# Kernel optimization log

Measured on AMD Instinct MI355X. Metric: run time of the kernel, lower is better.

Reference implementation:

```python
import jax, jax.numpy as jnp
import numpy as np

B, S, H = 2, 1024, 2048
HEADS = 16
QC = 1536      # q_compressed_dim
KVC = 512      # kv_compressed_dim
ROPE = 64      # qk_rope_dim
NOPE = H // HEADS  # 128, non-rope head dim
VH = 128       # v_head_dim
INTER = 1408   # MoE intermediate dim
NSH = 2        # shared experts
NRT = 8        # routed experts
TOPK = 2
EPS = 1e-6


def setup_inputs() -> dict:
    key = jax.random.key(0)
    ks = jax.random.split(key, 16)

    def w(k, shape, scale=0.02):
        return jax.random.normal(k, shape, jnp.float32) * scale

    return {
        "x": jax.random.normal(ks[0], (B, S, H), jnp.float32),
        "freq": jax.random.uniform(ks[1], (S, ROPE // 2), jnp.float32, 0.0, 2.0 * np.pi),
        "mask": jnp.zeros((S, S), jnp.float32),
        "w_attn_norm": jnp.ones((H,), jnp.float32),
        "w_ffn_norm": jnp.ones((H,), jnp.float32),
        "W_dq": w(ks[2], (H, QC)),
        "q_c_norm": jnp.ones((QC,), jnp.float32),
        "W_uq": w(ks[3], (QC, HEADS * (NOPE + ROPE))),
        "W_dkv": w(ks[4], (H, KVC + ROPE)),
        "kv_c_norm": jnp.ones((KVC,), jnp.float32),
        "W_ukv": w(ks[5], (KVC, HEADS * (NOPE + VH))),
        "W_o": w(ks[6], (HEADS * VH, H)),
        "W_r": w(ks[7], (H, NRT)),
        "Ws_gate": w(ks[8], (NSH, H, INTER)),
        "Ws_up": w(ks[9], (NSH, H, INTER)),
        "Ws_down": w(ks[10], (NSH, INTER, H)),
        "We_gate": w(ks[11], (NRT, H, INTER)),
        "We_up": w(ks[12], (NRT, H, INTER)),
        "We_down": w(ks[13], (NRT, INTER, H)),
    }


def rmsnorm(x, w):
    return x * jax.lax.rsqrt(jnp.mean(x * x, axis=-1, keepdims=True) + EPS) * w


def rope_apply(x, cos, sin):
    # x: [..., S, D]; cos/sin: [S, D/2], interleaved-pair rotation
    x1 = x[..., 0::2]
    x2 = x[..., 1::2]
    return jnp.stack([x1 * cos - x2 * sin, x1 * sin + x2 * cos], axis=-1).reshape(x.shape)


def _experts(t, Wg, Wu, Wd):
    # t: [T,H]; W*: [E,H,I]/[E,I,H] -> [E,T,H], SwiGLU per expert
    hid = jax.nn.silu(jnp.einsum('th,ehi->eti', t, Wg)) * jnp.einsum('th,ehi->eti', t, Wu)
    return jnp.einsum('eti,eih->eth', hid, Wd)


def reference(x, freq, mask, w_attn_norm, w_ffn_norm, W_dq, q_c_norm, W_uq, W_dkv,
              kv_c_norm, W_ukv, W_o, W_r, Ws_gate, Ws_up, Ws_down,
              We_gate, We_up, We_down):
    Bb, Ss, Hh = x.shape
    cos = jnp.cos(freq)
    sin = jnp.sin(freq)

    # ---- MLA attention (pre-norm) ----
    h = rmsnorm(x, w_attn_norm)
    cq = rmsnorm(h @ W_dq, q_c_norm)                              # [B,S,QC]
    q = (cq @ W_uq).reshape(Bb, Ss, HEADS, NOPE + ROPE).transpose(0, 2, 1, 3)
    q_nope, q_rope = q[..., :NOPE], q[..., NOPE:]
    q_rope = rope_apply(q_rope, cos, sin)                          # [B,Hh,S,ROPE]

    ckv = h @ W_dkv                                               # [B,S,KVC+ROPE]
    kv_c = rmsnorm(ckv[..., :KVC], kv_c_norm)
    k_rope = rope_apply(ckv[..., KVC:], cos, sin)                  # [B,S,ROPE] shared over heads
    kv = (kv_c @ W_ukv).reshape(Bb, Ss, HEADS, NOPE + VH).transpose(0, 2, 1, 3)
    k_nope, v = kv[..., :NOPE], kv[..., NOPE:]

    scale = 1.0 / np.sqrt(NOPE + ROPE)
    scores = (jnp.einsum('bhsd,bhtd->bhst', q_nope, k_nope)
              + jnp.einsum('bhsd,btd->bhst', q_rope, k_rope)) * scale + mask
    attn = jax.nn.softmax(scores, axis=-1)
    attn_out = jnp.einsum('bhst,bhtd->bshd', attn, v).reshape(Bb, Ss, HEADS * VH) @ W_o
    x = x + attn_out

    # ---- DeepSeekMoE FFN (pre-norm) ----
    t = rmsnorm(x, w_ffn_norm).reshape(Bb * Ss, Hh)
    shared = _experts(t, Ws_gate, Ws_up, Ws_down).sum(axis=0)      # [T,H]
    probs = jax.nn.softmax(t @ W_r, axis=-1)                       # [T,E]
    vals, idx = jax.lax.top_k(probs, TOPK)
    weights = (jax.nn.one_hot(idx, NRT, dtype=t.dtype) * vals[..., None]).sum(axis=1)  # [T,E]
    routed = jnp.einsum('eth,te->th', _experts(t, We_gate, We_up, We_down), weights)
    return x + (shared + routed).reshape(Bb, Ss, Hh)
```

## Files before the change

kernel.cpp:

```cpp
#include <hip/hip_runtime.h>

typedef __bf16 bf16;
typedef _Float16 f16;
typedef unsigned short u16;
typedef __bf16 bf16x8 __attribute__((ext_vector_type(8)));
typedef _Float16 f16x8 __attribute__((ext_vector_type(8)));
typedef unsigned short u16x8 __attribute__((ext_vector_type(8)));
typedef float f32x4 __attribute__((ext_vector_type(4)));

#define TOK   2048
#define SEQ   1024
#define HIDD  2048
#define NHEADS 16
#define QCD   1536
#define KVCD  512
#define ROPED 64
#define NOPED 128
#define QDIM  192
#define VHD   128
#define KVD   576
#define KVDP  640
#define INTERD 1408
#define GUD   2816
#define RMS_EPS 1e-6f
#define SPS   64.0f
#define OSC   (1.0f/4096.0f)

__device__ inline void split64(float v, f16& h, f16& l) {
    v *= SPS; h = (f16)v; l = (f16)(v - (float)h);
}

__device__ inline void gl_lds16(const void* g, void* l) {
    __builtin_amdgcn_global_load_lds(
        (const __attribute__((address_space(1))) void*)g,
        (__attribute__((address_space(3))) void*)l,
        16, 0, 0);
}

#define WAITN(N) asm volatile("s_waitcnt vmcnt(" #N ")" ::: "memory")

__global__ __launch_bounds__(256) void tconv_ex3_kernel(const float* __restrict__ gate,
                                                        const float* __restrict__ up,
                                                        const float* __restrict__ down,
                                                        bf16* __restrict__ dGU,
                                                        bf16* __restrict__ dD) {
    const float* src; bf16* dst; int K, N, rowMul, rowAdd;
    if (blockIdx.z == 0)      { src = gate; dst = dGU; K = HIDD;   N = INTERD; rowMul = 2; rowAdd = 0; }
    else if (blockIdx.z == 1) { src = up;   dst = dGU; K = HIDD;   N = INTERD; rowMul = 2; rowAdd = 1; }
    else                      { src = down; dst = dD;  K = INTERD; N = HIDD;   rowMul = 1; rowAdd = 0; }
    int nb = blockIdx.x * 32, kb = blockIdx.y * 32;
    if (nb >= N || kb >= K) return;
    __shared__ float tile[32][33];
    int tx = threadIdx.x & 31, ty = threadIdx.x >> 5;
#pragma unroll
    for (int i = 0; i < 32; i += 8)
        tile[ty + i][tx] = src[(long)(kb + ty + i) * N + nb + tx];
    __syncthreads();
#pragma unroll
    for (int i = 0; i < 32; i += 8) {
        int n = nb + ty + i;
        dst[(long)(n * rowMul + rowAdd) * K + kb + tx] = (bf16)tile[tx][ty + i];
    }
}

__global__ __launch_bounds__(256) void tconv_guall_kernel(const float* __restrict__ gate,
                                                          const float* __restrict__ up,
                                                          bf16* __restrict__ dstAll) {
    int e = blockIdx.z >> 1, isUp = blockIdx.z & 1;
    const float* src = (isUp ? up : gate) + (size_t)e * HIDD * INTERD;
    bf16* dst = dstAll + (size_t)e * GUD * HIDD;
    int nb = blockIdx.x * 32, kb = blockIdx.y * 32;
    __shared__ float tile[32][33];
    int tx = threadIdx.x & 31, ty = threadIdx.x >> 5;
#pragma unroll
    for (int i = 0; i < 32; i += 8)
        tile[ty + i][tx] = src[(long)(kb + ty + i) * INTERD + nb + tx];
    __syncthreads();
#pragma unroll
    for (int i = 0; i < 32; i += 8) {
        int n = nb + ty + i;
        dst[(long)(n * 2 + isUp) * HIDD + kb + tx] = (bf16)tile[tx][ty + i];
    }
}

__global__ __launch_bounds__(256) void tconv_downall_kernel(const float* __restrict__ down,
                                                            bf16* __restrict__ dstAll) {
    int e = blockIdx.z;
    const float* src = down + (size_t)e * INTERD * HIDD;
    bf16* dst = dstAll + (size_t)e * HIDD * INTERD;
    int nb = blockIdx.x * 32, kb = blockIdx.y * 32;
    __shared__ float tile[32][33];
    int tx = threadIdx.x & 31, ty = threadIdx.x >> 5;
#pragma unroll
    for (int i = 0; i < 32; i += 8)
        tile[ty + i][tx] = src[(long)(kb + ty + i) * HIDD + nb + tx];
    __syncthreads();
#pragma unroll
    for (int i = 0; i < 32; i += 8)
        dst[(long)(nb + ty + i) * INTERD + kb + tx] = (bf16)tile[tx][ty + i];
}

__global__ __launch_bounds__(256) void tconv3h_kernel(const float* __restrict__ src,
                                                      f16* __restrict__ dst,
                                                      int K, int N, int Npad) {
    __shared__ float tile[32][33];
    int nb = blockIdx.x * 32, kb = blockIdx.y * 32;
    int tx = threadIdx.x & 31, ty = threadIdx.x >> 5;
#pragma unroll
    for (int i = 0; i < 32; i += 8) {
        int k = kb + ty + i, n = nb + tx;
        tile[ty + i][tx] = (k < K && n < N) ? src[(long)k * N + n] : 0.f;
    }
    __syncthreads();
#pragma unroll
    for (int i = 0; i < 32; i += 8) {
        int n = nb + ty + i, k = kb + tx;
        if (n < Npad && k < K) {
            f16 h, l; split64(tile[tx][ty + i], h, l);
            long base = (long)n * (3 * K) + k;
            dst[base] = h; dst[base + K] = l; dst[base + 2 * K] = h;
        }
    }
}

template<int F16, int TM, int TN>
__global__ __launch_bounds__(256) void gemm_bt_kernel(
    const u16* __restrict__ A, const u16* __restrict__ B, void* __restrict__ Cv,
    const float* __restrict__ aux, const int* __restrict__ idx,
    const int* __restrict__ cntPtr,
    int K, int lda, int ldb, int ldc,
    long sA, long sB, long sC,
    int mode, int auxLd, float osc)
{
    constexpr int AM = TM / 32;
    constexpr int AN = TN / 32;
    constexpr int NBUF = (TM + TN > 192) ? 2 : 3;
    constexpr int PF = NBUF - 1;
    constexpr int L = TM / 32 + TN / 32;
    __shared__ u16 As[NBUF][TM * 64];
    __shared__ u16 Bs[NBUF][TN * 64];
    const int bn = blockIdx.x, bm = blockIdx.y, z = blockIdx.z;
    int cnt = 1 << 30;
    if (cntPtr) {
        cnt = cntPtr[z];
        int pad = (cnt + TM - 1) & ~(TM - 1);
        if (bm * TM >= pad) return;
    }
    const int tid = threadIdx.x, lane = tid & 63, w = tid >> 6;
    const int wm = w >> 1, wn = w & 1;
    const int lr = lane & 15;
    const int srow = lane >> 3, c16 = lane & 7;
    const u16* Ab = A + (long)z * sA + (long)bm * TM * lda;
    const u16* Bb = B + (long)z * sB + (long)bn * TN * ldb;
    f32x4 acc[AM][AN] = {};

    const bool aidx = (idx != nullptr && mode == 7);
    int iperm[4];
    if (aidx) {
#pragma unroll
        for (int i = 0; i < TM / 32; i++) {
            int r = bm * TM + i * 32 + w * 8 + srow;
            int v = idx[(long)z * TOK + r];
            iperm[i] = (r < cnt) ? v : 0;
        }
    }

    auto stage = [&](int buf, int k0) {
#pragma unroll
        for (int i = 0; i < TM / 32; i++) {
            int rb = i * 32 + w * 8;
            int row = rb + srow;
            int gc = ((c16 ^ (row & 7)) << 3);
            const u16* src = aidx ? (A + (long)iperm[i] * lda + k0 + gc)
                                  : (Ab + (long)row * lda + k0 + gc);
            gl_lds16(src, &As[buf][rb * 64]);
        }
#pragma unroll
        for (int i = 0; i < TN / 32; i++) {
            int rb = i * 32 + w * 8;
            int row = rb + srow;
            int gc = ((c16 ^ (row & 7)) << 3);
            gl_lds16(&Bb[(long)row * ldb + k0 + gc], &Bs[buf][rb * 64]);
        }
    };
    auto compute = [&](int cur) {
#pragma unroll
        for (int ks = 0; ks < 2; ks++) {
            u16x8 af[AM], bfr[AN];
#pragma unroll
            for (int mi = 0; mi < AM; mi++) {
                int row = wm * (TM / 2) + mi * 16 + lr;
                int cg = (ks * 4 + (lane >> 4)) ^ (row & 7);
                af[mi] = *(const u16x8*)&As[cur][row * 64 + cg * 8];
            }
#pragma unroll
            for (int ni = 0; ni < AN; ni++) {
                int row = wn * (TN / 2) + ni * 16 + lr;
                int cg = (ks * 4 + (lane >> 4)) ^ (row & 7);
                bfr[ni] = *(const u16x8*)&Bs[cur][row * 64 + cg * 8];
            }
#pragma unroll
            for (int mi = 0; mi < AM; mi++)
#pragma unroll
                for (int ni = 0; ni < AN; ni++) {
                    if constexpr (F16)
                        acc[mi][ni] = __builtin_amdgcn_mfma_f32_16x16x32_f16(
                            __builtin_bit_cast(f16x8, af[mi]),
                            __builtin_bit_cast(f16x8, bfr[ni]), acc[mi][ni], 0, 0, 0);
                    else
                        acc[mi][ni] = __builtin_amdgcn_mfma_f32_16x16x32_bf16(
                            __builtin_bit_cast(bf16x8, af[mi]),
                            __builtin_bit_cast(bf16x8, bfr[ni]), acc[mi][ni], 0, 0, 0);
                }
        }
    };

    const int nk = K >> 6;
#pragma unroll
    for (int p = 0; p < PF; ++p) if (p < nk) stage(p, p << 6);

    if constexpr (PF == 2) {
        for (int t = 0; t < nk; ++t) {
            if (t + PF < nk) stage((t + PF) % NBUF, (t + PF) << 6);
            const int inflight = (nk - 1 - t < PF) ? (nk - 1 - t) : PF;
            if (inflight >= 2) {
                if constexpr (L == 4) WAITN(8); else WAITN(12);
            } else if (inflight == 1) {
                if constexpr (L == 4) WAITN(4); else WAITN(6);
            } else {
                WAITN(0);
            }
            __builtin_amdgcn_s_barrier();
            __builtin_amdgcn_sched_barrier(0);
            compute(t % NBUF);
            __builtin_amdgcn_s_barrier();
        }
    } else {
        for (int t = 0; t < nk; ++t) {
            if (t + 1 < nk) stage((t + 1) & 1, (t + 1) << 6);
            if (t + 1 < nk) WAITN(8);
            else            WAITN(0);
            __builtin_amdgcn_s_barrier();
            __builtin_amdgcn_sched_barrier(0);
            compute(t & 1);
            __builtin_amdgcn_s_barrier();
        }
    }

    const int r0 = (lane >> 4) << 2;
    const int rowBase = bm * TM + wm * (TM / 2);
    const int colBase = bn * TN + wn * (TN / 2);
#pragma unroll
    for (int mi = 0; mi < AM; mi++) {
#pragma unroll
        for (int ni = 0; ni < AN; ni++) {
#pragma unroll
            for (int r = 0; r < 4; r++) {
                int row = rowBase + mi * 16 + r0 + r;
                int col = colBase + ni * 16 + lr;
                float val = acc[mi][ni][r] * osc;
                long ci = (long)z * sC + (long)row * ldc + col;
                if (mode == 0) {
                    ((float*)Cv)[ci] = val;
                } else if (mode == 2) {
                    ((float*)Cv)[ci] = val + aux[(long)row * auxLd + col];
                } else if (mode == 3) {
                    float s = aux ? aux[(long)row * auxLd] : 1.f;
                    ((float*)Cv)[ci] += s * val;
                } else if (mode == 5) {
                    if (row < cnt) {
                        int tok = idx[(long)z * TOK + row];
                        atomicAdd(&((float*)Cv)[(long)tok * ldc + col],
                                  aux[(long)tok * auxLd + z] * val);
                    }
                } else if (mode == 7) {
                    float other = __shfl_xor(val, 1, 64);
                    if (!(lane & 1)) {
                        float g = val, u = other;
                        ((bf16*)Cv)[(long)z * sC + (long)row * auxLd + (col >> 1)] =
                            (bf16)(g / (1.f + expf(-g)) * u);
                    }
                } else {
                    f16 h = (f16)val; f16 l = (f16)(val - (float)h);
                    ((f16*)Cv)[ci] = h; ((f16*)Cv)[ci + auxLd] = h; ((f16*)Cv)[ci + 2 * auxLd] = l;
                }
            }
        }
    }
}

__global__ __launch_bounds__(256) void rmsnorm_kernel(const float* __restrict__ in,
                                                      const float* __restrict__ w,
                                                      bf16* __restrict__ outB,
                                                      float* __restrict__ copyOut, int C) {
    long row = blockIdx.x;
    const float* r = in + row * C;
    float ss = 0.f;
    for (int i = threadIdx.x; i < C; i += 256) { float v = r[i]; ss += v * v; }
    for (int off = 32; off > 0; off >>= 1) ss += __shfl_down(ss, off, 64);
    __shared__ float red[5];
    int lane = threadIdx.x & 63, wv = threadIdx.x >> 6;
    if (lane == 0) red[wv] = ss;
    __syncthreads();
    if (threadIdx.x == 0) red[4] = rsqrtf((red[0] + red[1] + red[2] + red[3]) / C + RMS_EPS);
    __syncthreads();
    float sc = red[4];
    for (int i = threadIdx.x; i < C; i += 256) {
        outB[row * C + i] = (bf16)(r[i] * sc * w[i]);
        if (copyOut) copyOut[row * C + i] = r[i];
    }
}

__global__ __launch_bounds__(256) void rmsnorm3h_kernel(const float* __restrict__ in,
                                                        const float* __restrict__ w,
                                                        f16* __restrict__ out3, int C) {
    long row = blockIdx.x;
    const float* r = in + row * C;
    float ss = 0.f;
    for (int i = threadIdx.x; i < C; i += 256) { float v = r[i]; ss += v * v; }
    for (int off = 32; off > 0; off >>= 1) ss += __shfl_down(ss, off, 64);
    __shared__ float red[5];
    int lane = threadIdx.x & 63, wv = threadIdx.x >> 6;
    if (lane == 0) red[wv] = ss;
    __syncthreads();
    if (threadIdx.x == 0) red[4] = rsqrtf((red[0] + red[1] + red[2] + red[3]) / C + RMS_EPS);
    __syncthreads();
    float sc = red[4];
    f16* o = out3 + row * (3L * C);
    for (int i = threadIdx.x; i < C; i += 256) {
        f16 h, l; split64(r[i] * sc * w[i], h, l);
        o[i] = h; o[C + i] = h; o[2 * C + i] = l;
    }
}

__global__ __launch_bounds__(256) void kvsplit3h_kernel(const float* __restrict__ ckv,
                                                        const float* __restrict__ nrm,
                                                        const float* __restrict__ freq,
                                                        f16* __restrict__ kvc3,
                                                        float* __restrict__ krope) {
    int t = blockIdx.x; int s = t & (SEQ - 1);
    const float* r = ckv + (long)t * KVDP;
    float ss = 0.f;
    for (int i = threadIdx.x; i < KVCD; i += 256) { float v = r[i]; ss += v * v; }
    for (int off = 32; off > 0; off >>= 1) ss += __shfl_down(ss, off, 64);
    __shared__ float red[5];
    int lane = threadIdx.x & 63, wv = threadIdx.x >> 6;
    if (lane == 0) red[wv] = ss;
    __syncthreads();
    if (threadIdx.x == 0) red[4] = rsqrtf((red[0] + red[1] + red[2] + red[3]) / KVCD + RMS_EPS);
    __syncthreads();
    float sc = red[4];
    f16* o = kvc3 + (long)t * (3 * KVCD);
    for (int i = threadIdx.x; i < KVCD; i += 256) {
        f16 h, l; split64(r[i] * sc * nrm[i], h, l);
        o[i] = h; o[KVCD + i] = h; o[2 * KVCD + i] = l;
    }
    if (threadIdx.x < 32) {
        int i = threadIdx.x;
        float f = freq[s * 32 + i], c = cosf(f), sn = sinf(f);
        float x1 = r[KVCD + 2 * i], x2 = r[KVCD + 2 * i + 1];
        krope[(long)t * ROPED + 2 * i]     = x1 * c - x2 * sn;
        krope[(long)t * ROPED + 2 * i + 1] = x1 * sn + x2 * c;
    }
}

__global__ __launch_bounds__(256) void build_q3h_kernel(const float* __restrict__ qpre,
                                                        const float* __restrict__ freq,
                                                        f16* __restrict__ q3) {
    int t = blockIdx.x; int b = t >> 10, s = t & (SEQ - 1);
    for (int idx = threadIdx.x; idx < NHEADS * 96; idx += 256) {
        int h = idx / 96, j = idx % 96;
        const float* qrow = qpre + (long)t * 3072 + h * QDIM;
        f16* dst = q3 + ((long)(b * NHEADS + h) * SEQ + s) * (3 * QDIM);
        if (j < 64) {
            int d = 2 * j;
#pragma unroll
            for (int u = 0; u < 2; u++) {
                f16 hh, ll; split64(qrow[d + u], hh, ll);
                dst[d + u] = hh; dst[QDIM + d + u] = hh; dst[2 * QDIM + d + u] = ll;
            }
        } else {
            int i = j - 64;
            float f = freq[s * 32 + i], c = cosf(f), sn = sinf(f);
            float x1 = qrow[NOPED + 2 * i], x2 = qrow[NOPED + 2 * i + 1];
            float v0 = x1 * c - x2 * sn, v1 = x1 * sn + x2 * c;
            int d = NOPED + 2 * i;
            f16 h0, l0, h1, l1; split64(v0, h0, l0); split64(v1, h1, l1);
            dst[d] = h0; dst[QDIM + d] = h0; dst[2 * QDIM + d] = l0;
            dst[d + 1] = h1; dst[QDIM + d + 1] = h1; dst[2 * QDIM + d + 1] = l1;
        }
    }
}

__global__ __launch_bounds__(256) void build_k3h_kernel(const float* __restrict__ kv,
                                                        const float* __restrict__ krope,
                                                        f16* __restrict__ k3,
                                                        f16* __restrict__ v3T) {
    int t = blockIdx.x; int b = t >> 10, s = t & (SEQ - 1);
    const float* kvrow = kv + (long)t * 4096;
    const float* kr = krope + (long)t * ROPED;
    for (int idx = threadIdx.x; idx < NHEADS * 96; idx += 256) {
        int h = idx / 96, j = idx % 96;
        f16* dst = k3 + ((long)(b * NHEADS + h) * SEQ + s) * (3 * QDIM);
        float v0, v1; int d;
        if (j < 64) { d = 2 * j; v0 = kvrow[h * 256 + d]; v1 = kvrow[h * 256 + d + 1]; }
        else { int i = j - 64; d = NOPED + 2 * i; v0 = kr[2 * i]; v1 = kr[2 * i + 1]; }
        f16 h0, l0, h1, l1; split64(v0, h0, l0); split64(v1, h1, l1);
        dst[d] = h0; dst[QDIM + d] = l0; dst[2 * QDIM + d] = h0;
        dst[d + 1] = h1; dst[QDIM + d + 1] = l1; dst[2 * QDIM + d + 1] = h1;
    }
    for (int idx = threadIdx.x; idx < NHEADS * VHD; idx += 256) {
        int h = idx >> 7, d = idx & 127;
        f16 hh, ll; split64(kvrow[h * 256 + NOPED + d], hh, ll);
        long base = ((long)(b * NHEADS + h) * VHD + d) * (3 * SEQ) + s;
        v3T[base] = hh; v3T[base + SEQ] = ll; v3T[base + 2 * SEQ] = hh;
    }
}

__global__ __launch_bounds__(256) void softmax3h_kernel(const float* __restrict__ scores,
                                                        const float* __restrict__ mask,
                                                        f16* __restrict__ P3, float scale) {
    int s = blockIdx.x, h = blockIdx.y;
    const float* row  = scores + ((long)h * SEQ + s) * SEQ;
    const float* mrow = mask + (long)s * SEQ;
    f16* prow = P3 + ((long)h * SEQ + s) * (3 * SEQ);
    float v[4]; float m = -1e30f;
#pragma unroll
    for (int j = 0; j < 4; j++) {
        int i = threadIdx.x + j * 256;
        v[j] = row[i] * scale + mrow[i];
        m = fmaxf(m, v[j]);
    }
    for (int off = 32; off > 0; off >>= 1) m = fmaxf(m, __shfl_down(m, off, 64));
    __shared__ float redm[5], reds[5];
    int lane = threadIdx.x & 63, wv = threadIdx.x >> 6;
    if (lane == 0) redm[wv] = m;
    __syncthreads();
    if (threadIdx.x == 0) redm[4] = fmaxf(fmaxf(redm[0], redm[1]), fmaxf(redm[2], redm[3]));
    __syncthreads();
    float M = redm[4];
    float sum = 0.f;
#pragma unroll
    for (int j = 0; j < 4; j++) { v[j] = expf(v[j] - M); sum += v[j]; }
    for (int off = 32; off > 0; off >>= 1) sum += __shfl_down(sum, off, 64);
    if (lane == 0) reds[wv] = sum;
    __syncthreads();
    if (threadIdx.x == 0) reds[4] = reds[0] + reds[1] + reds[2] + reds[3];
    __syncthreads();
    float inv = 1.f / reds[4];
#pragma unroll
    for (int j = 0; j < 4; j++) {
        int i = threadIdx.x + j * 256;
        f16 hh, ll; split64(v[j] * inv, hh, ll);
        prow[i] = hh; prow[SEQ + i] = hh; prow[2 * SEQ + i] = ll;
    }
}

__global__ void zero_counts_kernel(int* counts) {
    if (threadIdx.x < 8) counts[threadIdx.x] = 0;
}

__global__ __launch_bounds__(64) void router_kernel(const float* __restrict__ x2,
                                                    const float* __restrict__ wffn,
                                                    const float* __restrict__ Wr,
                                                    float* __restrict__ wts,
                                                    int* __restrict__ perm,
                                                    int* __restrict__ counts) {
    int t = blockIdx.x; int lane = threadIdx.x;
    const float* r = x2 + (long)t * HIDD;
    float ss = 0.f;
    for (int k = lane; k < HIDD; k += 64) { float v = r[k]; ss += v * v; }
    for (int off = 32; off > 0; off >>= 1) ss += __shfl_down(ss, off, 64);
    float sc = rsqrtf(__shfl(ss, 0, 64) / HIDD + RMS_EPS);
    float acc[8] = {0, 0, 0, 0, 0, 0, 0, 0};
    for (int k = lane; k < HIDD; k += 64) {
        float tv = r[k] * sc * wffn[k];
        const float* wr = Wr + (long)k * 8;
#pragma unroll
        for (int e = 0; e < 8; e++) acc[e] += tv * wr[e];
    }
#pragma unroll
    for (int e = 0; e < 8; e++)
        for (int off = 32; off > 0; off >>= 1) acc[e] += __shfl_down(acc[e], off, 64);
    if (lane == 0) {
        float m = acc[0];
#pragma unroll
        for (int e = 1; e < 8; e++) m = fmaxf(m, acc[e]);
        float p[8]; float se = 0.f;
#pragma unroll
        for (int e = 0; e < 8; e++) { p[e] = expf(acc[e] - m); se += p[e]; }
        float inv = 1.f / se;
        int i1 = 0; float v1 = p[0];
        for (int e = 1; e < 8; e++) if (p[e] > v1) { v1 = p[e]; i1 = e; }
        int i2 = -1; float v2 = -1.f;
        for (int e = 0; e < 8; e++) if (e != i1 && p[e] > v2) { v2 = p[e]; i2 = e; }
#pragma unroll
        for (int e = 0; e < 8; e++)
            wts[(long)t * 8 + e] = (e == i1) ? v1 * inv : ((e == i2) ? v2 * inv : 0.f);
        int s1 = atomicAdd(&counts[i1], 1); perm[i1 * TOK + s1] = t;
        int s2 = atomicAdd(&counts[i2], 1); perm[i2 * TOK + s2] = t;
    }
}

static inline size_t alignup(size_t v) { return (v + 255) & ~(size_t)255; }

extern "C" void kernel_launch(void* const* d_in, const int* in_sizes, int n_in,
                              void* d_out, int out_size, void* d_ws, size_t ws_size,
                              hipStream_t stream) {
    const float* x       = (const float*)d_in[0];
    const float* freq    = (const float*)d_in[1];
    const float* mask    = (const float*)d_in[2];
    const float* w_attn  = (const float*)d_in[3];
    const float* w_ffn   = (const float*)d_in[4];
    const float* W_dq    = (const float*)d_in[5];
    const float* q_c_nrm = (const float*)d_in[6];
    const float* W_uq    = (const float*)d_in[7];
    const float* W_dkv   = (const float*)d_in[8];
    const float* kv_nrm  = (const float*)d_in[9];
    const float* W_ukv   = (const float*)d_in[10];
    const float* W_o     = (const float*)d_in[11];
    const float* W_r     = (const float*)d_in[12];
    const float* Ws_gate = (const float*)d_in[13];
    const float* Ws_up   = (const float*)d_in[14];
    const float* Ws_down = (const float*)d_in[15];
    const float* We_gate = (const float*)d_in[16];
    const float* We_up   = (const float*)d_in[17];
    const float* We_down = (const float*)d_in[18];
    float* out = (float*)d_out;
    char* ws = (char*)d_ws;
    (void)in_sizes; (void)n_in; (void)out_size;

    size_t o = 0;
    auto alloc = [&](size_t n) { size_t r = o; o += alignup(n); return r; };
    size_t oWslot = alloc((size_t)3072 * 3 * QCD * 2);
    size_t oQ3    = alloc((size_t)32 * SEQ * 3 * QDIM * 2);
    size_t oK3    = alloc((size_t)32 * SEQ * 3 * QDIM * 2);
    size_t oV3T   = alloc((size_t)32 * VHD * 3 * SEQ * 2);
    size_t oAttn3 = alloc((size_t)TOK * 3 * HIDD * 2);
    size_t oX2    = alloc((size_t)TOK * HIDD * 4);
    size_t oTbuf  = alloc((size_t)TOK * HIDD * 2);
    size_t oWts   = alloc((size_t)TOK * 8 * 4);
    size_t oPerm  = alloc((size_t)8 * TOK * 4);
    size_t oCnt   = alloc((size_t)8 * 4);
    size_t oKrope = alloc((size_t)TOK * ROPED * 4);
    size_t zH3   = alignup((size_t)TOK * 3 * HIDD * 2);
    size_t zCqp  = alignup((size_t)TOK * QCD * 4);
    size_t zCq3  = alignup((size_t)TOK * 3 * QCD * 2);
    size_t zQp   = alignup((size_t)TOK * 3072 * 4);
    size_t zCkv  = alignup((size_t)TOK * KVDP * 4);
    size_t zKvc3 = alignup((size_t)TOK * 3 * KVCD * 2);
    size_t zKv   = alignup((size_t)TOK * 4096 * 4);
    size_t chain = zH3 + zCqp + zCq3 + zQp + zCkv + zKvc3 + zKv;
    size_t zScores = alignup((size_t)16 * SEQ * SEQ * 4);
    size_t zP3     = alignup((size_t)16 * SEQ * 3 * SEQ * 2);
    size_t zHid8   = alignup((size_t)8 * TOK * INTERD * 2);
    size_t zWegu   = alignup((size_t)8 * GUD * HIDD * 2);
    size_t arenaSz = chain;
    if (zScores + zP3 > arenaSz) arenaSz = zScores + zP3;
    if (zHid8 + zWegu > arenaSz) arenaSz = zHid8 + zWegu;
    size_t oArena = alloc(arenaSz);
    if (ws_size < o) return;

    size_t oH3   = oArena;
    size_t oCqp  = oH3 + zH3;
    size_t oCq3  = oCqp + zCqp;
    size_t oQp   = oCq3 + zCq3;
    size_t oCkv  = oQp + zQp;
    size_t oKvc3 = oCkv + zCkv;
    size_t oKv   = oKvc3 + zKvc3;
    size_t oScores = oArena;
    size_t oP3     = oArena + zScores;
    size_t oHid8   = oArena;
    size_t oWegu   = oArena + zHid8;

    f16*  wslotH = (f16*)(ws + oWslot);
    bf16* wslotB = (bf16*)(ws + oWslot);
    bf16* wslotB2 = (bf16*)(ws + oWslot + (size_t)GUD * HIDD * 2);
    f16*  q3    = (f16*)(ws + oQ3);
    f16*  k3    = (f16*)(ws + oK3);
    f16*  v3T   = (f16*)(ws + oV3T);
    f16*  attn3 = (f16*)(ws + oAttn3);
    float* x2   = (float*)(ws + oX2);
    bf16* tbuf  = (bf16*)(ws + oTbuf);
    float* wts  = (float*)(ws + oWts);
    int*  perm  = (int*)(ws + oPerm);
    int*  counts = (int*)(ws + oCnt);
    float* krope = (float*)(ws + oKrope);
    f16*  h3    = (f16*)(ws + oH3);
    float* cqpre = (float*)(ws + oCqp);
    f16*  cq3   = (f16*)(ws + oCq3);
    float* qpre = (float*)(ws + oQp);
    float* ckv  = (float*)(ws + oCkv);
    f16*  kvc3  = (f16*)(ws + oKvc3);
    float* kv   = (float*)(ws + oKv);
    float* scores = (float*)(ws + oScores);
    f16*  P3    = (f16*)(ws + oP3);
    bf16* hid8  = (bf16*)(ws + oHid8);
    bf16* WeguAll = (bf16*)(ws + oWegu);
    bf16* WedAll  = (bf16*)(ws + oWegu);

    auto tconv3h = [&](const float* src, f16* dst, int K, int N, int Npad) {
        dim3 g((Npad + 31) / 32, (K + 31) / 32);
        tconv3h_kernel<<<g, 256, 0, stream>>>(src, dst, K, N, Npad);
    };
    auto tconvEx = [&](const float* gate, const float* up, const float* down) {
        tconv_ex3_kernel<<<dim3(64, 64, 3), 256, 0, stream>>>(gate, up, down, wslotB, wslotB2);
    };
    auto gH128x128 = [&](const f16* A, const f16* B, void* C, const float* aux,
                         int M, int N, int K, int lda, int ldb, int ldc,
                         long sA, long sB, long sC, int Z, int mode, int auxLd, float osc) {
        dim3 g(N / 128, M / 128, Z);
        gemm_bt_kernel<1, 128, 128><<<g, 256, 0, stream>>>((const u16*)A, (const u16*)B, C, aux,
            nullptr, nullptr, K, lda, ldb, ldc, sA, sB, sC, mode, auxLd, osc);
    };
    auto gH128x64 = [&](const f16* A, const f16* B, void* C, const float* aux,
                        int M, int N, int K, int lda, int ldb, int ldc,
                        long sA, long sB, long sC, int Z, int mode, int auxLd, float osc) {
        dim3 g(N / 64, M / 128, Z);
        gemm_bt_kernel<1, 128, 64><<<g, 256, 0, stream>>>((const u16*)A, (const u16*)B, C, aux,
            nullptr, nullptr, K, lda, ldb, ldc, sA, sB, sC, mode, auxLd, osc);
    };
    auto gH64x64 = [&](const f16* A, const f16* B, void* C, const float* aux,
                       int M, int N, int K, int lda, int ldb, int ldc,
                       long sA, long sB, long sC, int Z, int mode, int auxLd, float osc) {
        dim3 g(N / 64, M / 64, Z);
        gemm_bt_kernel<1, 64, 64><<<g, 256, 0, stream>>>((const u16*)A, (const u16*)B, C, aux,
            nullptr, nullptr, K, lda, ldb, ldc, sA, sB, sC, mode, auxLd, osc);
    };
    auto gB128x64 = [&](const bf16* A, const bf16* B, void* C,
                        const float* aux, const int* idx, const int* cnt,
                        int M, int N, int K, int lda, int ldb, int ldc, int mode, int auxLd) {
        dim3 g(N / 64, M / 128, 1);
        gemm_bt_kernel<0, 128, 64><<<g, 256, 0, stream>>>((const u16*)A, (const u16*)B, C, aux,
            idx, cnt, K, lda, ldb, ldc, 0, 0, 0, mode, auxLd, 1.0f);
    };

    rmsnorm3h_kernel<<<TOK, 256, 0, stream>>>(x, w_attn, h3, HIDD);

    tconv3h(W_dq, wslotH, HIDD, QCD, QCD);
    gH128x64(h3, wslotH, cqpre, nullptr, TOK, QCD, 3 * HIDD, 3 * HIDD, 3 * HIDD, QCD,
             0, 0, 0, 1, 0, 0, OSC);
    rmsnorm3h_kernel<<<TOK, 256, 0, stream>>>(cqpre, q_c_nrm, cq3, QCD);

    tconv3h(W_uq, wslotH, QCD, 3072, 3072);
    gH128x128(cq3, wslotH, qpre, nullptr, TOK, 3072, 3 * QCD, 3 * QCD, 3 * QCD, 3072,
              0, 0, 0, 1, 0, 0, OSC);

    tconv3h(W_dkv, wslotH, HIDD, KVD, KVDP);
    gH64x64(h3, wslotH, ckv, nullptr, TOK, KVDP, 3 * HIDD, 3 * HIDD, 3 * HIDD, KVDP,
            0, 0, 0, 1, 0, 0, OSC);
    kvsplit3h_kernel<<<TOK, 256, 0, stream>>>(ckv, kv_nrm, freq, kvc3, krope);

    tconv3h(W_ukv, wslotH, KVCD, 4096, 4096);
    gH128x128(kvc3, wslotH, kv, nullptr, TOK, 4096, 3 * KVCD, 3 * KVCD, 3 * KVCD, 4096,
              0, 0, 0, 1, 0, 0, OSC);

    build_q3h_kernel<<<TOK, 256, 0, stream>>>(qpre, freq, q3);
    build_k3h_kernel<<<TOK, 256, 0, stream>>>(kv, krope, k3, v3T);

    for (int b = 0; b < 2; b++) {
        int h0 = b * NHEADS;
        gH128x128(q3 + (size_t)h0 * SEQ * 3 * QDIM, k3 + (size_t)h0 * SEQ * 3 * QDIM,
                  scores, nullptr, SEQ, SEQ, 3 * QDIM, 3 * QDIM, 3 * QDIM, SEQ,
                  (long)SEQ * 3 * QDIM, (long)SEQ * 3 * QDIM, (long)SEQ * SEQ, 16, 0, 0, OSC);
        softmax3h_kernel<<<dim3(SEQ, 16), 256, 0, stream>>>(scores, mask, P3,
                                                            1.f / sqrtf((float)QDIM));
        gH64x64(P3, v3T + (size_t)h0 * VHD * 3 * SEQ,
                attn3 + (size_t)b * SEQ * 3 * HIDD, nullptr,
                SEQ, VHD, 3 * SEQ, 3 * SEQ, 3 * SEQ, 3 * HIDD,
                (long)SEQ * 3 * SEQ, (long)VHD * 3 * SEQ, (long)VHD, 16, 6, HIDD,
                1.0f / SPS);
    }

    tconv3h(W_o, wslotH, HIDD, HIDD, HIDD);
    gH128x64(attn3, wslotH, x2, x, TOK, HIDD, 3 * HIDD, 3 * HIDD, 3 * HIDD, HIDD,
             0, 0, 0, 1, 2, HIDD, OSC);

    rmsnorm_kernel<<<TOK, 256, 0, stream>>>(x2, w_ffn, tbuf, out, HIDD);
    zero_counts_kernel<<<1, 64, 0, stream>>>(counts);
    router_kernel<<<TOK, 64, 0, stream>>>(x2, w_ffn, W_r, wts, perm, counts);

    for (int e = 0; e < 2; e++) {
        tconvEx(Ws_gate + (size_t)e * HIDD * INTERD,
                Ws_up   + (size_t)e * HIDD * INTERD,
                Ws_down + (size_t)e * INTERD * HIDD);
        gB128x64(tbuf, wslotB, hid8, nullptr, nullptr, nullptr,
                 TOK, GUD, HIDD, HIDD, HIDD, GUD, 7, INTERD);
        gB128x64(hid8, wslotB2, out, nullptr, nullptr, nullptr,
                 TOK, HIDD, INTERD, INTERD, INTERD, HIDD, 3, 0);
    }

    tconv_guall_kernel<<<dim3(INTERD / 32, HIDD / 32, 16), 256, 0, stream>>>(
        We_gate, We_up, WeguAll);
    {
        dim3 g(GUD / 64, TOK / 64, 8);
        gemm_bt_kernel<0, 64, 64><<<g, 256, 0, stream>>>(
            (const u16*)tbuf, (const u16*)WeguAll, hid8, nullptr, perm, counts,
            HIDD, HIDD, HIDD, 0, 0, (long)GUD * HIDD, (long)TOK * INTERD, 7, INTERD, 1.0f);
    }
    tconv_downall_kernel<<<dim3(HIDD / 32, INTERD / 32, 8), 256, 0, stream>>>(
        We_down, WedAll);
    {
        dim3 g(HIDD / 64, TOK / 64, 8);
        gemm_bt_kernel<0, 64, 64><<<g, 256, 0, stream>>>(
            (const u16*)hid8, (const u16*)WedAll, out, wts, perm, counts,
            INTERD, INTERD, INTERD, HIDD, (long)TOK * INTERD, (long)HIDD * INTERD, 0,
            5, 8, 1.0f);
    }
}
```

Baseline: 1.390 ms.

## Batch shared experts and use a compact tile plan for routed MoE GEMMs

The two shared experts now run as single batched launches (z=2): one weight transpose for both experts, one gate/up GEMM and one down GEMM. The down GEMM accumulates into the output with float atomics. The routed experts' grid, previously padded to 8 experts times all token tiles, becomes a compact list of (expert, row block) pairs built on device by a new plan kernel, and uses 128x64 tiles. The aim is fewer launches and fewer idle early-exiting blocks. In exchange it adds atomic contention on the output, a serial single-thread plan kernel, and the total tile count is assumed never to exceed MAXPLAN.

```diff
diff --git a/kernel.cpp b/kernel.cpp
--- a/kernel.cpp
+++ b/kernel.cpp
@@ -25,6 +25,7 @@
 #define RMS_EPS 1e-6f
 #define SPS   64.0f
 #define OSC   (1.0f/4096.0f)
+#define MAXPLAN 40
 
 __device__ inline void split64(float v, f16& h, f16& l) {
     v *= SPS; h = (f16)v; l = (f16)(v - (float)h);
@@ -38,30 +39,6 @@
 }
 
 #define WAITN(N) asm volatile("s_waitcnt vmcnt(" #N ")" ::: "memory")
-
-__global__ __launch_bounds__(256) void tconv_ex3_kernel(const float* __restrict__ gate,
-                                                        const float* __restrict__ up,
-                                                        const float* __restrict__ down,
-                                                        bf16* __restrict__ dGU,
-                                                        bf16* __restrict__ dD) {
-    const float* src; bf16* dst; int K, N, rowMul, rowAdd;
-    if (blockIdx.z == 0)      { src = gate; dst = dGU; K = HIDD;   N = INTERD; rowMul = 2; rowAdd = 0; }
-    else if (blockIdx.z == 1) { src = up;   dst = dGU; K = HIDD;   N = INTERD; rowMul = 2; rowAdd = 1; }
-    else                      { src = down; dst = dD;  K = INTERD; N = HIDD;   rowMul = 1; rowAdd = 0; }
-    int nb = blockIdx.x * 32, kb = blockIdx.y * 32;
-    if (nb >= N || kb >= K) return;
-    __shared__ float tile[32][33];
-    int tx = threadIdx.x & 31, ty = threadIdx.x >> 5;
-#pragma unroll
-    for (int i = 0; i < 32; i += 8)
-        tile[ty + i][tx] = src[(long)(kb + ty + i) * N + nb + tx];
-    __syncthreads();
-#pragma unroll
-    for (int i = 0; i < 32; i += 8) {
-        int n = nb + ty + i;
-        dst[(long)(n * rowMul + rowAdd) * K + kb + tx] = (bf16)tile[tx][ty + i];
-    }
-}
 
 __global__ __launch_bounds__(256) void tconv_guall_kernel(const float* __restrict__ gate,
                                                           const float* __restrict__ up,
@@ -123,11 +100,24 @@
     }
 }
 
+__global__ void plan_kernel(const int* __restrict__ counts, int* __restrict__ plan,
+                            int* __restrict__ planCnt) {
+    if (threadIdx.x == 0) {
+        int p = 0;
+        for (int e = 0; e < 8; e++) {
+            int c = counts[e];
+            for (int rb = 0; rb < c; rb += 128) { plan[2 * p] = e; plan[2 * p + 1] = rb; p++; }
+        }
+        planCnt[0] = p;
+    }
+}
+
 template<int F16, int TM, int TN>
 __global__ __launch_bounds__(256) void gemm_bt_kernel(
     const u16* __restrict__ A, const u16* __restrict__ B, void* __restrict__ Cv,
     const float* __restrict__ aux, const int* __restrict__ idx,
     const int* __restrict__ cntPtr,
+    const int* __restrict__ plan, const int* __restrict__ planCnt,
     int K, int lda, int ldb, int ldc,
     long sA, long sB, long sC,
     int mode, int auxLd, float osc)
@@ -139,27 +129,37 @@
     constexpr int L = TM / 32 + TN / 32;
     __shared__ u16 As[NBUF][TM * 64];
     __shared__ u16 Bs[NBUF][TN * 64];
-    const int bn = blockIdx.x, bm = blockIdx.y, z = blockIdx.z;
+    const int bn = blockIdx.x;
+    int z = blockIdx.z;
+    int rowBase;
     int cnt = 1 << 30;
-    if (cntPtr) {
+    if (plan) {
+        int pb = blockIdx.y;
+        if (pb >= planCnt[0]) return;
+        z = plan[2 * pb]; rowBase = plan[2 * pb + 1];
         cnt = cntPtr[z];
-        int pad = (cnt + TM - 1) & ~(TM - 1);
-        if (bm * TM >= pad) return;
+    } else {
+        rowBase = blockIdx.y * TM;
+        if (cntPtr) {
+            cnt = cntPtr[z];
+            int pad = (cnt + TM - 1) & ~(TM - 1);
+            if (rowBase >= pad) return;
+        }
     }
     const int tid = threadIdx.x, lane = tid & 63, w = tid >> 6;
     const int wm = w >> 1, wn = w & 1;
     const int lr = lane & 15;
     const int srow = lane >> 3, c16 = lane & 7;
-    const u16* Ab = A + (long)z * sA + (long)bm * TM * lda;
+    const u16* Ab = A + (long)z * sA + (long)rowBase * lda;
     const u16* Bb = B + (long)z * sB + (long)bn * TN * ldb;
     f32x4 acc[AM][AN] = {};
 
     const bool aidx = (idx != nullptr && mode == 7);
-    int iperm[4];
+    int iperm[TM / 32];
     if (aidx) {
 #pragma unroll
         for (int i = 0; i < TM / 32; i++) {
-            int r = bm * TM + i * 32 + w * 8 + srow;
+            int r = rowBase + i * 32 + w * 8 + srow;
             int v = idx[(long)z * TOK + r];
             iperm[i] = (r < cnt) ? v : 0;
         }
@@ -248,7 +248,7 @@
     }
 
     const int r0 = (lane >> 4) << 2;
-    const int rowBase = bm * TM + wm * (TM / 2);
+    const int rowB = rowBase + wm * (TM / 2);
     const int colBase = bn * TN + wn * (TN / 2);
 #pragma unroll
     for (int mi = 0; mi < AM; mi++) {
@@ -256,7 +256,7 @@
         for (int ni = 0; ni < AN; ni++) {
 #pragma unroll
             for (int r = 0; r < 4; r++) {
-                int row = rowBase + mi * 16 + r0 + r;
+                int row = rowB + mi * 16 + r0 + r;
                 int col = colBase + ni * 16 + lr;
                 float val = acc[mi][ni][r] * osc;
                 long ci = (long)z * sC + (long)row * ldc + col;
@@ -280,6 +280,8 @@
                         ((bf16*)Cv)[(long)z * sC + (long)row * auxLd + (col >> 1)] =
                             (bf16)(g / (1.f + expf(-g)) * u);
                     }
+                } else if (mode == 8) {
+                    atomicAdd(&((float*)Cv)[(long)row * ldc + col], val);
                 } else {
                     f16 h = (f16)val; f16 l = (f16)(val - (float)h);
                     ((f16*)Cv)[ci] = h; ((f16*)Cv)[ci + auxLd] = h; ((f16*)Cv)[ci + 2 * auxLd] = l;
@@ -542,6 +544,7 @@
     size_t oWts   = alloc((size_t)TOK * 8 * 4);
     size_t oPerm  = alloc((size_t)8 * TOK * 4);
     size_t oCnt   = alloc((size_t)8 * 4);
+    size_t oPlan  = alloc((size_t)(2 * MAXPLAN + 1) * 4);
     size_t oKrope = alloc((size_t)TOK * ROPED * 4);
     size_t zH3   = alignup((size_t)TOK * 3 * HIDD * 2);
     size_t zCqp  = alignup((size_t)TOK * QCD * 4);
@@ -574,8 +577,6 @@
     size_t oWegu   = oArena + zHid8;
 
     f16*  wslotH = (f16*)(ws + oWslot);
-    bf16* wslotB = (bf16*)(ws + oWslot);
-    bf16* wslotB2 = (bf16*)(ws + oWslot + (size_t)GUD * HIDD * 2);
     f16*  q3    = (f16*)(ws + oQ3);
     f16*  k3    = (f16*)(ws + oK3);
     f16*  v3T   = (f16*)(ws + oV3T);
@@ -585,6 +586,8 @@
     float* wts  = (float*)(ws + oWts);
     int*  perm  = (int*)(ws + oPerm);
     int*  counts = (int*)(ws + oCnt);
+    int*  plan  = (int*)(ws + oPlan);
+    int*  planCnt = plan + 2 * MAXPLAN;
     float* krope = (float*)(ws + oKrope);
     f16*  h3    = (f16*)(ws + oH3);
     float* cqpre = (float*)(ws + oCqp);
@@ -598,41 +601,33 @@
     bf16* hid8  = (bf16*)(ws + oHid8);
     bf16* WeguAll = (bf16*)(ws + oWegu);
     bf16* WedAll  = (bf16*)(ws + oWegu);
+    bf16* WsguAll = (bf16*)(ws + oWegu);
+    bf16* WsdAll  = (bf16*)(ws + oWegu + (size_t)2 * GUD * HIDD * 2);
 
     auto tconv3h = [&](const float* src, f16* dst, int K, int N, int Npad) {
         dim3 g((Npad + 31) / 32, (K + 31) / 32);
         tconv3h_kernel<<<g, 256, 0, stream>>>(src, dst, K, N, Npad);
-    };
-    auto tconvEx = [&](const float* gate, const float* up, const float* down) {
-        tconv_ex3_kernel<<<dim3(64, 64, 3), 256, 0, stream>>>(gate, up, down, wslotB, wslotB2);
     };
     auto gH128x128 = [&](const f16* A, const f16* B, void* C, const float* aux,
                          int M, int N, int K, int lda, int ldb, int ldc,
                          long sA, long sB, long sC, int Z, int mode, int auxLd, float osc) {
         dim3 g(N / 128, M / 128, Z);
         gemm_bt_kernel<1, 128, 128><<<g, 256, 0, stream>>>((const u16*)A, (const u16*)B, C, aux,
-            nullptr, nullptr, K, lda, ldb, ldc, sA, sB, sC, mode, auxLd, osc);
+            nullptr, nullptr, nullptr, nullptr, K, lda, ldb, ldc, sA, sB, sC, mode, auxLd, osc);
     };
     auto gH128x64 = [&](const f16* A, const f16* B, void* C, const float* aux,
                         int M, int N, int K, int lda, int ldb, int ldc,
                         long sA, long sB, long sC, int Z, int mode, int auxLd, float osc) {
         dim3 g(N / 64, M / 128, Z);
         gemm_bt_kernel<1, 128, 64><<<g, 256, 0, stream>>>((const u16*)A, (const u16*)B, C, aux,
-            nullptr, nullptr, K, lda, ldb, ldc, sA, sB, sC, mode, auxLd, osc);
+            nullptr, nullptr, nullptr, nullptr, K, lda, ldb, ldc, sA, sB, sC, mode, auxLd, osc);
     };
     auto gH64x64 = [&](const f16* A, const f16* B, void* C, const float* aux,
                        int M, int N, int K, int lda, int ldb, int ldc,
                        long sA, long sB, long sC, int Z, int mode, int auxLd, float osc) {
         dim3 g(N / 64, M / 64, Z);
         gemm_bt_kernel<1, 64, 64><<<g, 256, 0, stream>>>((const u16*)A, (const u16*)B, C, aux,
-            nullptr, nullptr, K, lda, ldb, ldc, sA, sB, sC, mode, auxLd, osc);
-    };
-    auto gB128x64 = [&](const bf16* A, const bf16* B, void* C,
-                        const float* aux, const int* idx, const int* cnt,
-                        int M, int N, int K, int lda, int ldb, int ldc, int mode, int auxLd) {
-        dim3 g(N / 64, M / 128, 1);
-        gemm_bt_kernel<0, 128, 64><<<g, 256, 0, stream>>>((const u16*)A, (const u16*)B, C, aux,
-            idx, cnt, K, lda, ldb, ldc, 0, 0, 0, mode, auxLd, 1.0f);
+            nullptr, nullptr, nullptr, nullptr, K, lda, ldb, ldc, sA, sB, sC, mode, auxLd, osc);
     };
 
     rmsnorm3h_kernel<<<TOK, 256, 0, stream>>>(x, w_attn, h3, HIDD);
@@ -679,32 +674,43 @@
     rmsnorm_kernel<<<TOK, 256, 0, stream>>>(x2, w_ffn, tbuf, out, HIDD);
     zero_counts_kernel<<<1, 64, 0, stream>>>(counts);
     router_kernel<<<TOK, 64, 0, stream>>>(x2, w_ffn, W_r, wts, perm, counts);
-
-    for (int e = 0; e < 2; e++) {
-        tconvEx(Ws_gate + (size_t)e * HIDD * INTERD,
-                Ws_up   + (size_t)e * HIDD * INTERD,
-                Ws_down + (size_t)e * INTERD * HIDD);
-        gB128x64(tbuf, wslotB, hid8, nullptr, nullptr, nullptr,
-                 TOK, GUD, HIDD, HIDD, HIDD, GUD, 7, INTERD);
-        gB128x64(hid8, wslotB2, out, nullptr, nullptr, nullptr,
-                 TOK, HIDD, INTERD, INTERD, INTERD, HIDD, 3, 0);
+    plan_kernel<<<1, 64, 0, stream>>>(counts, plan, planCnt);
+
+    tconv_guall_kernel<<<dim3(INTERD / 32, HIDD / 32, 4), 256, 0, stream>>>(
+        Ws_gate, Ws_up, WsguAll);
+    tconv_downall_kernel<<<dim3(HIDD / 32, INTERD / 32, 2), 256, 0, stream>>>(
+        Ws_down, WsdAll);
+    {
+        dim3 g(GUD / 64, TOK / 128, 2);
+        gemm_bt_kernel<0, 128, 64><<<g, 256, 0, stream>>>(
+            (const u16*)tbuf, (const u16*)WsguAll, hid8, nullptr, nullptr, nullptr,
+            nullptr, nullptr, HIDD, HIDD, HIDD, 0,
+            0, (long)GUD * HIDD, (long)TOK * INTERD, 7, INTERD, 1.0f);
+    }
+    {
+        dim3 g(HIDD / 64, TOK / 128, 2);
+        gemm_bt_kernel<0, 128, 64><<<g, 256, 0, stream>>>(
+            (const u16*)hid8, (const u16*)WsdAll, out, nullptr, nullptr, nullptr,
+            nullptr, nullptr, INTERD, INTERD, INTERD, HIDD,
+            (long)TOK * INTERD, (long)HIDD * INTERD, 0, 8, 0, 1.0f);
     }
 
     tconv_guall_kernel<<<dim3(INTERD / 32, HIDD / 32, 16), 256, 0, stream>>>(
         We_gate, We_up, WeguAll);
     {
-        dim3 g(GUD / 64, TOK / 64, 8);
-        gemm_bt_kernel<0, 64, 64><<<g, 256, 0, stream>>>(
+        dim3 g(GUD / 64, MAXPLAN, 1);
+        gemm_bt_kernel<0, 128, 64><<<g, 256, 0, stream>>>(
             (const u16*)tbuf, (const u16*)WeguAll, hid8, nullptr, perm, counts,
-            HIDD, HIDD, HIDD, 0, 0, (long)GUD * HIDD, (long)TOK * INTERD, 7, INTERD, 1.0f);
+            plan, planCnt, HIDD, HIDD, HIDD, 0,
+            0, (long)GUD * HIDD, (long)TOK * INTERD, 7, INTERD, 1.0f);
     }
     tconv_downall_kernel<<<dim3(HIDD / 32, INTERD / 32, 8), 256, 0, stream>>>(
         We_down, WedAll);
     {
-        dim3 g(HIDD / 64, TOK / 64, 8);
-        gemm_bt_kernel<0, 64, 64><<<g, 256, 0, stream>>>(
+        dim3 g(HIDD / 64, MAXPLAN, 1);
+        gemm_bt_kernel<0, 128, 64><<<g, 256, 0, stream>>>(
             (const u16*)hid8, (const u16*)WedAll, out, wts, perm, counts,
-            INTERD, INTERD, INTERD, HIDD, (long)TOK * INTERD, (long)HIDD * INTERD, 0,
-            5, 8, 1.0f);
-    }
-}
+            plan, planCnt, INTERD, INTERD, INTERD, HIDD,
+            (long)TOK * INTERD, (long)HIDD * INTERD, 0, 5, 8, 1.0f);
+    }
+}
```

New measurement: 1.436 ms. +3.3%, slower.
